# Performance work log

Measured on AMD Instinct MI355X. Metric: run time of the kernel, lower is better.

Reference implementation:

```python
import jax, jax.numpy as jnp
import numpy as np

N = 8192      # input_dim (graph nodes)
H = 256       # hidden_dim
KN = 128      # kernel_num
B = 2048      # batch size
W = 2 * H + 2 # conv kernel width


def setup_inputs() -> dict:
    key = jax.random.key(0)
    ks = jax.random.split(key, 10)
    a = float(np.sqrt(6.0 / (N + H)))  # xavier_uniform bound
    embedding = jax.random.uniform(ks[0], (N, H), minval=-a, maxval=a, dtype=jnp.float32)
    A = jax.random.normal(ks[1], (N, N), dtype=jnp.float32) * 0.01  # dense adjacency
    k1 = jax.random.normal(ks[2], (KN, 1, 1, W), dtype=jnp.float32) * 0.05  # filter_size=1
    b1 = jax.random.normal(ks[3], (KN,), dtype=jnp.float32) * 0.05
    k2 = jax.random.normal(ks[4], (KN, 1, 2, W), dtype=jnp.float32) * 0.05  # filter_size=2
    b2 = jax.random.normal(ks[5], (KN,), dtype=jnp.float32) * 0.05
    dense_w = jax.random.normal(ks[6], (2, KN * 4), dtype=jnp.float32) * 0.02
    dense_b = jax.random.normal(ks[7], (2,), dtype=jnp.float32) * 0.02
    batch_x = jax.random.randint(ks[8], (B,), 0, N)
    batch_y = jax.random.randint(ks[9], (B,), 0, N)
    return {"embedding": embedding, "A": A, "k1": k1, "b1": b1, "k2": k2,
            "b2": b2, "dense_w": dense_w, "dense_b": dense_b,
            "batch_x": batch_x, "batch_y": batch_y}


def _encode(t, kern, bias):
    # t: [B,1,1,2H]; Conv2d padding=1 both dims, kernel (f, 2H+2) -> out [B,KN,4-f,1]
    out = jax.lax.conv_general_dilated(
        t, kern, window_strides=(1, 1), padding=((1, 1), (1, 1)),
        dimension_numbers=("NCHW", "OIHW", "NCHW"))
    out = jax.nn.relu(out + bias[None, :, None, None])
    return jnp.max(out, axis=(2, 3))  # max_pool2d over full height, width==1 -> [B,KN]


def reference(embedding, A, k1, b1, k2, b2, dense_w, dense_b, batch_x, batch_y):
    # GCN layer (featureless): layer1 = A @ embedding, shape [N,H]
    layer1 = jnp.matmul(A, embedding)
    # Record path (the only path feeding the output): rQ=layer1[bx], rA=layer1[by];
    # ErQ = rA, ErA = rQ per the torch soft_attention record bookkeeping.
    rQ = layer1[batch_x]  # [B,H]
    rA = layer1[batch_y]  # [B,H]
    d = rQ - rA
    tq = d * d            # (rQ-ErQ)^2 == (rA-ErA)^2, symmetric
    mul = rQ * rA         # rQ*ErQ == rA*ErA
    t = jnp.concatenate([tq, mul], axis=1)[:, None, None, :]  # [B,1,1,2H]
    enc = jnp.concatenate([_encode(t, k1, b1), _encode(t, k2, b2)], axis=1)  # [B,2*KN]
    q_re = jax.nn.relu(enc)  # dropout is identity in eval mode
    a_re = q_re              # a-side computation is algebraically identical (symmetry above)
    re = jnp.concatenate([q_re, a_re], axis=1)  # [B,4*KN]
    score = jnp.matmul(re, dense_w.T) + dense_b  # [B,2]
    return jax.nn.log_softmax(score, axis=1)
```

## Files before the change

kernel.cpp:

```cpp
#include <hip/hip_runtime.h>
#include <stdint.h>
#include <math.h>

#define NN 8192
#define HD 256
#define BATCH 2048
#define KSPLIT 16
#define KCH (NN / KSPLIT)

typedef __attribute__((ext_vector_type(8))) short bf16x8;
typedef __attribute__((ext_vector_type(4))) float f32x4;

static __device__ __forceinline__ uint32_t pack_bf2(float x, float y) {
  union { float f; uint32_t u; } a, b; a.f = x; b.f = y;
  uint32_t ua = a.u + 0x7FFFu + ((a.u >> 16) & 1u);
  uint32_t ub = b.u + 0x7FFFu + ((b.u >> 16) & 1u);
  return (ua >> 16) | (ub & 0xFFFF0000u);
}
static __device__ __forceinline__ float bf_lo(uint32_t u) {
  return __uint_as_float(u << 16);
}
static __device__ __forceinline__ float bf_hi(uint32_t u) {
  return __uint_as_float(u & 0xFFFF0000u);
}

extern "C" __global__ void k_prep(const float* __restrict__ emb,
                                  const float* __restrict__ k1,
                                  const float* __restrict__ k2,
                                  uint16_t* __restrict__ Bm,
                                  uint16_t* __restrict__ Wm) {
  const int tid = threadIdx.x;
  if (blockIdx.x < 256) {
    __shared__ float ts[32][257];
    const int kc = blockIdx.x;
#pragma unroll
    for (int i = 0; i < 32; i++)
      ts[i][tid] = emb[(size_t)(kc * 32 + i) * HD + tid];
    __syncthreads();
#pragma unroll
    for (int c = 0; c < 4; c++) {
      int e = c * 256 + tid;
      int ci = e >> 6, l = e & 63;
      int g = l >> 4, col = ci * 16 + (l & 15);
      uint4 v;
      v.x = pack_bf2(ts[g * 8 + 0][col], ts[g * 8 + 1][col]);
      v.y = pack_bf2(ts[g * 8 + 2][col], ts[g * 8 + 3][col]);
      v.z = pack_bf2(ts[g * 8 + 4][col], ts[g * 8 + 5][col]);
      v.w = pack_bf2(ts[g * 8 + 6][col], ts[g * 8 + 7][col]);
      ((uint4*)Bm)[(size_t)kc * 1024 + e] = v;
    }
  } else {
    const int c = (blockIdx.x - 256) * 256 + tid;
    const int lcl = c & 63;
    const int ci = (c >> 6) % 24;
    const int kc = c / (24 * 64);
    const int j = ci * 16 + (lcl & 15);
    const int k0 = kc * 32 + ((lcl >> 4) << 3);
    float f[8];
#pragma unroll
    for (int jj = 0; jj < 8; jj++) {
      int k = k0 + jj;
      f[jj] = (j < 128) ? k1[j * 514 + 1 + k]
            : (j < 256) ? k2[(j - 128) * 1028 + 515 + k]
                        : k2[(j - 256) * 1028 + 1 + k];
    }
    uint4 v;
    v.x = pack_bf2(f[0], f[1]); v.y = pack_bf2(f[2], f[3]);
    v.z = pack_bf2(f[4], f[5]); v.w = pack_bf2(f[6], f[7]);
    *(uint4*)(Wm + (size_t)c * 8) = v;
  }
}

extern "C" __global__ __launch_bounds__(256, 2)
void k_gemm(const float* __restrict__ A, const uint16_t* __restrict__ Bm,
            const int* __restrict__ bx, const int* __restrict__ by,
            uint16_t* __restrict__ Rp) {
  __shared__ __align__(16) uint16_t Asm[64 * 512];
  const int tid = threadIdx.x;
  const int kblk = blockIdx.x & 15;
  const int mblk = blockIdx.x >> 4;
  const int wv = tid >> 6, l = tid & 63, g = l >> 4, l15 = l & 15;

  {
    const int r = tid >> 2, b = tid & 3;
    const int gr = mblk * 64 + r;
    const int arow = (gr < BATCH) ? bx[gr] : by[gr - BATCH];
    const float* aSrc = A + (size_t)arow * NN + (size_t)kblk * KCH + b * 4;
    const int ris = r >> 4, l15s = r & 15;
    const int joff = (b & 1) << 2;
    const int gb = b >> 1;
#pragma unroll
    for (int half = 0; half < 2; ++half) {
      float4 t[16];
#pragma unroll
      for (int m16 = 0; m16 < 16; ++m16)
        t[m16] = *(const float4*)(aSrc + (half * 16 + m16) * 16);
#pragma unroll
      for (int m16 = 0; m16 < 16; ++m16) {
        const int m = half * 16 + m16;
        const int kc = m >> 1;
        const int gg = ((m & 1) << 1) + gb;
        const int off = ((kc * 4 + ris) * 64 + gg * 16 + l15s) * 8 + joff;
        uint2 v;
        v.x = pack_bf2(t[m16].x, t[m16].y);
        v.y = pack_bf2(t[m16].z, t[m16].w);
        *(uint2*)(Asm + off) = v;
      }
    }
  }
  __syncthreads();

  f32x4 acc[4][4] = {};
  const uint16_t* bWave = Bm + (((size_t)(kblk * 16) * 16 + wv * 4) * 64 + l) * 8;
#pragma unroll 4
  for (int kc = 0; kc < 16; ++kc) {
    bf16x8 bfr[4];
#pragma unroll
    for (int cj = 0; cj < 4; ++cj)
      bfr[cj] = *(const bf16x8*)(bWave + ((size_t)kc * 16 + cj) * 512);
    bf16x8 af[4];
#pragma unroll
    for (int ri = 0; ri < 4; ++ri)
      af[ri] = *(const bf16x8*)(Asm + (size_t)((kc * 4 + ri) * 64 + l) * 8);
#pragma unroll
    for (int ri = 0; ri < 4; ++ri)
#pragma unroll
      for (int cj = 0; cj < 4; ++cj)
        acc[ri][cj] = __builtin_amdgcn_mfma_f32_16x16x32_bf16(
            af[ri], bfr[cj], acc[ri][cj], 0, 0, 0);
  }
  __syncthreads();

  uint16_t* Ct = Asm;
#pragma unroll
  for (int ri = 0; ri < 4; ri++)
#pragma unroll
    for (int cj = 0; cj < 4; cj++)
#pragma unroll
      for (int r = 0; r < 4; r++) {
        float v = acc[ri][cj][r];
        float vn = __shfl_xor(v, 1);
        if ((l15 & 1) == 0) {
          int row16 = ri * 16 + g * 4 + r;
          int col = wv * 64 + cj * 16 + l15;
          *(uint32_t*)(Ct + row16 * 256 + col) = pack_bf2(v, vn);
        }
      }
  __syncthreads();
  {
    const int row2 = tid >> 2, cb = (tid & 3) * 64;
    const uint4* src = (const uint4*)(Ct + row2 * 256 + cb);
    uint16_t* dst = Rp + ((size_t)kblk * 4096 + mblk * 64 + row2) * HD + cb;
    uint4 v0 = src[0], v1 = src[1], v2 = src[2], v3 = src[3];
    ((uint4*)dst)[0] = v0; ((uint4*)dst)[1] = v1;
    ((uint4*)dst)[2] = v2; ((uint4*)dst)[3] = v3;
  }
}

extern "C" __global__ __launch_bounds__(256, 2)
void k_tail(const uint16_t* __restrict__ Rp, const uint16_t* __restrict__ Wm,
            const float* __restrict__ b1, const float* __restrict__ b2,
            const float* __restrict__ dw, const float* __restrict__ dbias,
            float* __restrict__ out) {
  __shared__ __align__(16) uint16_t t_frag[16 * 64 * 8];
  __shared__ float Cl[8][388];
  __shared__ float coef[6][128];
  const int tid = threadIdx.x;
  const int b0 = blockIdx.x * 8;
  const int wv = tid >> 6, l = tid & 63, g = l >> 4, l15 = l & 15;
  if (tid < 128) {
    coef[0][tid] = dw[tid] + dw[256 + tid];
    coef[1][tid] = dw[128 + tid] + dw[384 + tid];
    coef[2][tid] = dw[512 + tid] + dw[768 + tid];
    coef[3][tid] = dw[640 + tid] + dw[896 + tid];
    coef[4][tid] = b1[tid];
    coef[5][tid] = b2[tid];
  }
  {
    const int r = tid >> 5, c8 = (tid & 31) * 8;
    float rq[8] = {}, ra[8] = {};
#pragma unroll
    for (int p = 0; p < KSPLIT; p++) {
      uint4 q4 = *(const uint4*)(Rp + ((size_t)p * 4096 + b0 + r) * HD + c8);
      uint4 a4 = *(const uint4*)(Rp + ((size_t)p * 4096 + BATCH + b0 + r) * HD + c8);
      const uint32_t* qw = (const uint32_t*)&q4;
      const uint32_t* aw = (const uint32_t*)&a4;
#pragma unroll
      for (int w = 0; w < 4; w++) {
        rq[2 * w] += bf_lo(qw[w]); rq[2 * w + 1] += bf_hi(qw[w]);
        ra[2 * w] += bf_lo(aw[w]); ra[2 * w + 1] += bf_hi(aw[w]);
      }
    }
    uint32_t tq[4], ml[4];
#pragma unroll
    for (int w = 0; w < 4; w++) {
      float d0 = rq[2 * w] - ra[2 * w], d1 = rq[2 * w + 1] - ra[2 * w + 1];
      tq[w] = pack_bf2(d0 * d0, d1 * d1);
      ml[w] = pack_bf2(rq[2 * w] * ra[2 * w], rq[2 * w + 1] * ra[2 * w + 1]);
    }
    const int kc1 = c8 >> 5, gm = (c8 >> 3) & 3;
    const int kc2 = 8 + kc1;
    *(uint4*)(t_frag + (kc1 * 64 + gm * 16 + r) * 8) = *(uint4*)tq;
    *(uint4*)(t_frag + (kc2 * 64 + gm * 16 + r) * 8) = *(uint4*)ml;
    uint4 z = {0, 0, 0, 0};
    *(uint4*)(t_frag + (kc1 * 64 + gm * 16 + 8 + r) * 8) = z;
    *(uint4*)(t_frag + (kc2 * 64 + gm * 16 + 8 + r) * 8) = z;
  }
  __syncthreads();
  {
    f32x4 acc[6] = {};
    const uint16_t* wB = Wm + ((size_t)(wv * 6) * 64 + l) * 8;
#pragma unroll 2
    for (int kc = 0; kc < 16; kc++) {
      bf16x8 af = *(const bf16x8*)(t_frag + (kc * 64 + l) * 8);
#pragma unroll
      for (int ci = 0; ci < 6; ci++) {
        bf16x8 w = *(const bf16x8*)(wB + (size_t)kc * 12288 + ci * 512);
        acc[ci] = __builtin_amdgcn_mfma_f32_16x16x32_bf16(af, w, acc[ci], 0, 0, 0);
      }
    }
#pragma unroll
    for (int ci = 0; ci < 6; ci++)
#pragma unroll
      for (int r = 0; r < 4; r++) {
        int row16 = g * 4 + r;
        if (row16 < 8) Cl[row16][wv * 96 + ci * 16 + l15] = acc[ci][r];
      }
  }
  __syncthreads();
  {
    const int r = tid >> 5, ch0 = (tid & 31) * 4;
    float s0 = 0.f, s1 = 0.f;
#pragma unroll
    for (int cc = 0; cc < 4; cc++) {
      const int c = ch0 + cc;
      float d1 = Cl[r][c], d2a = Cl[r][128 + c], d2b = Cl[r][256 + c];
      float bb1 = coef[4][c], bb2 = coef[5][c];
      float e1 = fmaxf(0.f, fmaxf(bb1, d1 + bb1));
      float e2 = fmaxf(0.f, fmaxf(d2a + bb2, d2b + bb2));
      s0 += e1 * coef[0][c] + e2 * coef[1][c];
      s1 += e1 * coef[2][c] + e2 * coef[3][c];
    }
#pragma unroll
    for (int off = 16; off >= 1; off >>= 1) {
      s0 += __shfl_xor(s0, off, 32);
      s1 += __shfl_xor(s1, off, 32);
    }
    if ((tid & 31) == 0) {
      s0 += dbias[0]; s1 += dbias[1];
      float m = fmaxf(s0, s1);
      float lse = m + logf(expf(s0 - m) + expf(s1 - m));
      out[(b0 + r) * 2] = s0 - lse;
      out[(b0 + r) * 2 + 1] = s1 - lse;
    }
  }
}

extern "C" void kernel_launch(void* const* d_in, const int* in_sizes, int n_in,
                              void* d_out, int out_size, void* d_ws, size_t ws_size,
                              hipStream_t stream) {
  const float* emb = (const float*)d_in[0];
  const float* A   = (const float*)d_in[1];
  const float* k1  = (const float*)d_in[2];
  const float* b1  = (const float*)d_in[3];
  const float* k2  = (const float*)d_in[4];
  const float* b2  = (const float*)d_in[5];
  const float* dw  = (const float*)d_in[6];
  const float* dbi = (const float*)d_in[7];
  const int* bx = (const int*)d_in[8];
  const int* by = (const int*)d_in[9];
  float* out = (float*)d_out;
  char* ws = (char*)d_ws;
  uint16_t* Bm = (uint16_t*)ws;
  uint16_t* Wm = (uint16_t*)(ws + (4u << 20));
  uint16_t* Rp = (uint16_t*)(ws + (8u << 20));

  k_prep<<<352, 256, 0, stream>>>(emb, k1, k2, Bm, Wm);
  k_gemm<<<64 * KSPLIT, 256, 0, stream>>>(A, Bm, bx, by, Rp);
  k_tail<<<256, 256, 0, stream>>>(Rp, Wm, b1, b2, dw, dbi, out);
}
```

Before: 72.27 us.

## Halve K-split and prefetch second K stage of gathered A during MFMA

```diff
diff --git a/kernel.cpp b/kernel.cpp
--- a/kernel.cpp
+++ b/kernel.cpp
@@ -5,7 +5,7 @@
 #define NN 8192
 #define HD 256
 #define BATCH 2048
-#define KSPLIT 16
+#define KSPLIT 8
 #define KCH (NN / KSPLIT)
 
 typedef __attribute__((ext_vector_type(8))) short bf16x8;
@@ -77,58 +77,71 @@
             uint16_t* __restrict__ Rp) {
   __shared__ __align__(16) uint16_t Asm[64 * 512];
   const int tid = threadIdx.x;
-  const int kblk = blockIdx.x & 15;
-  const int mblk = blockIdx.x >> 4;
+  const int kblk = blockIdx.x & 7;
+  const int mblk = blockIdx.x >> 3;
   const int wv = tid >> 6, l = tid & 63, g = l >> 4, l15 = l & 15;
 
-  {
-    const int r = tid >> 2, b = tid & 3;
-    const int gr = mblk * 64 + r;
-    const int arow = (gr < BATCH) ? bx[gr] : by[gr - BATCH];
-    const float* aSrc = A + (size_t)arow * NN + (size_t)kblk * KCH + b * 4;
-    const int ris = r >> 4, l15s = r & 15;
-    const int joff = (b & 1) << 2;
-    const int gb = b >> 1;
-#pragma unroll
-    for (int half = 0; half < 2; ++half) {
-      float4 t[16];
-#pragma unroll
-      for (int m16 = 0; m16 < 16; ++m16)
-        t[m16] = *(const float4*)(aSrc + (half * 16 + m16) * 16);
-#pragma unroll
-      for (int m16 = 0; m16 < 16; ++m16) {
-        const int m = half * 16 + m16;
-        const int kc = m >> 1;
-        const int gg = ((m & 1) << 1) + gb;
-        const int off = ((kc * 4 + ris) * 64 + gg * 16 + l15s) * 8 + joff;
-        uint2 v;
-        v.x = pack_bf2(t[m16].x, t[m16].y);
-        v.y = pack_bf2(t[m16].z, t[m16].w);
-        *(uint2*)(Asm + off) = v;
-      }
-    }
+  const int r = tid >> 2, b = tid & 3;
+  const int gr = mblk * 64 + r;
+  const int arow = (gr < BATCH) ? bx[gr] : by[gr - BATCH];
+  const float* aSrc = A + (size_t)arow * NN + (size_t)kblk * KCH + b * 4;
+  const int ris = r >> 4, l15s = r & 15;
+  const int joff = (b & 1) << 2;
+  const int gb = b >> 1;
+
+#define PACK1(v_, m_) { \
+    const int kcp = (m_) >> 1; \
+    const int gg = (((m_) & 1) << 1) + gb; \
+    const int off = ((kcp * 4 + ris) * 64 + gg * 16 + l15s) * 8 + joff; \
+    uint2 u_; u_.x = pack_bf2((v_).x, (v_).y); u_.y = pack_bf2((v_).z, (v_).w); \
+    *(uint2*)(Asm + off) = u_; }
+
+#pragma unroll
+  for (int half = 0; half < 2; ++half) {
+    float4 t[16];
+#pragma unroll
+    for (int m16 = 0; m16 < 16; ++m16)
+      t[m16] = *(const float4*)(aSrc + (half * 16 + m16) * 16);
+#pragma unroll
+    for (int m16 = 0; m16 < 16; ++m16) PACK1(t[m16], half * 16 + m16);
   }
   __syncthreads();
 
   f32x4 acc[4][4] = {};
-  const uint16_t* bWave = Bm + (((size_t)(kblk * 16) * 16 + wv * 4) * 64 + l) * 8;
-#pragma unroll 4
-  for (int kc = 0; kc < 16; ++kc) {
-    bf16x8 bfr[4];
-#pragma unroll
-    for (int cj = 0; cj < 4; ++cj)
-      bfr[cj] = *(const bf16x8*)(bWave + ((size_t)kc * 16 + cj) * 512);
-    bf16x8 af[4];
-#pragma unroll
-    for (int ri = 0; ri < 4; ++ri)
-      af[ri] = *(const bf16x8*)(Asm + (size_t)((kc * 4 + ri) * 64 + l) * 8);
-#pragma unroll
-    for (int ri = 0; ri < 4; ++ri)
-#pragma unroll
-      for (int cj = 0; cj < 4; ++cj)
-        acc[ri][cj] = __builtin_amdgcn_mfma_f32_16x16x32_bf16(
-            af[ri], bfr[cj], acc[ri][cj], 0, 0, 0);
-  }
+  const uint16_t* bWave = Bm + (((size_t)(kblk * 32) * 16 + wv * 4) * 64 + l) * 8;
+
+#define COMPUTE_RANGE(stage, kc0, kc1) \
+  _Pragma("unroll") \
+  for (int kc = (kc0); kc < (kc1); ++kc) { \
+    bf16x8 bfr[4]; \
+    _Pragma("unroll") \
+    for (int cj = 0; cj < 4; ++cj) \
+      bfr[cj] = *(const bf16x8*)(bWave + (((stage) * 16 + kc) * 16 + cj) * 512); \
+    _Pragma("unroll") \
+    for (int ri = 0; ri < 4; ++ri) { \
+      bf16x8 af = *(const bf16x8*)(Asm + (size_t)((kc * 4 + ri) * 64 + l) * 8); \
+      _Pragma("unroll") \
+      for (int cj = 0; cj < 4; ++cj) \
+        acc[ri][cj] = __builtin_amdgcn_mfma_f32_16x16x32_bf16( \
+            af, bfr[cj], acc[ri][cj], 0, 0, 0); } }
+
+  float4 s2a[16];
+#pragma unroll
+  for (int m = 0; m < 16; ++m)
+    s2a[m] = *(const float4*)(aSrc + 512 + m * 16);
+  COMPUTE_RANGE(0, 0, 8)
+  float4 s2b[16];
+#pragma unroll
+  for (int m = 0; m < 16; ++m)
+    s2b[m] = *(const float4*)(aSrc + 512 + (16 + m) * 16);
+  COMPUTE_RANGE(0, 8, 16)
+  __syncthreads();
+#pragma unroll
+  for (int m = 0; m < 16; ++m) PACK1(s2a[m], m)
+#pragma unroll
+  for (int m = 0; m < 16; ++m) PACK1(s2b[m], 16 + m)
+  __syncthreads();
+  COMPUTE_RANGE(1, 0, 16)
   __syncthreads();
 
   uint16_t* Ct = Asm;
@@ -137,11 +150,11 @@
 #pragma unroll
     for (int cj = 0; cj < 4; cj++)
 #pragma unroll
-      for (int r = 0; r < 4; r++) {
-        float v = acc[ri][cj][r];
+      for (int rr = 0; rr < 4; rr++) {
+        float v = acc[ri][cj][rr];
         float vn = __shfl_xor(v, 1);
         if ((l15 & 1) == 0) {
-          int row16 = ri * 16 + g * 4 + r;
+          int row16 = ri * 16 + g * 4 + rr;
           int col = wv * 64 + cj * 16 + l15;
           *(uint32_t*)(Ct + row16 * 256 + col) = pack_bf2(v, vn);
         }
@@ -155,6 +168,8 @@
     ((uint4*)dst)[0] = v0; ((uint4*)dst)[1] = v1;
     ((uint4*)dst)[2] = v2; ((uint4*)dst)[3] = v3;
   }
+#undef PACK1
+#undef COMPUTE_RANGE
 }
 
 extern "C" __global__ __launch_bounds__(256, 2)
@@ -222,9 +237,9 @@
 #pragma unroll
     for (int ci = 0; ci < 6; ci++)
 #pragma unroll
-      for (int r = 0; r < 4; r++) {
-        int row16 = g * 4 + r;
-        if (row16 < 8) Cl[row16][wv * 96 + ci * 16 + l15] = acc[ci][r];
+      for (int rr = 0; rr < 4; rr++) {
+        int row16 = g * 4 + rr;
+        if (row16 < 8) Cl[row16][wv * 96 + ci * 16 + l15] = acc[ci][rr];
       }
   }
   __syncthreads();
```

Result: faster. 61.23 us (-15.3%).
